# Performance work log

Measured on AMD Instinct MI355X. Metric: run time of the kernel, lower is better.

The kernel has to match this reference:

```python
import jax, jax.numpy as jnp
import numpy as np

REMOVE_FACTOR = 1000000.0


def setup_inputs() -> dict:
    key = jax.random.key(0)
    ks = jax.random.split(key, 6)
    B, Te, Td = 4, 512, 128
    D_en, D_de, U = 256, 512, 128
    en_seq = jax.random.normal(ks[0], (B, Te, D_en), dtype=jnp.float32)
    de_seq = jax.random.normal(ks[1], (B, Td, D_de), dtype=jnp.float32)
    mask = jax.random.randint(ks[2], (B, Te), 0, 2).astype(jnp.int32)
    w_en = jax.random.normal(ks[3], (D_en, U), dtype=jnp.float32) * (1.0 / np.sqrt(D_en))
    w_de = jax.random.normal(ks[4], (D_de, U), dtype=jnp.float32) * (1.0 / np.sqrt(D_de))
    nu = jax.random.normal(ks[5], (U, 1), dtype=jnp.float32) * (1.0 / np.sqrt(U))
    return {"en_seq": en_seq, "de_seq": de_seq, "mask": mask,
            "w_en": w_en, "w_de": w_de, "nu": nu}


def reference(en_seq, de_seq, mask, w_en, w_de, nu):
    # en_seq: [B,Te,D_en], de_seq: [B,Td,D_de], mask: [B,Te] (0/1)
    m = mask.astype(en_seq.dtype)
    en = en_seq * m[..., None]                         # masked encoder states
    en_p = jnp.einsum('bte,eu->btu', en, w_en)          # [B,Te,U]
    de_p = jnp.einsum('bdf,fu->bdu', de_seq, w_de)      # [B,Td,U]
    # additive (Bahdanau) scores: scores[b,td,te] = tanh(en_p[te]+de_p[td]) @ nu
    h = jnp.tanh(en_p[:, None, :, :] + de_p[:, :, None, :])  # [B,Td,Te,U]
    mu = jnp.einsum('bdtu,u->bdt', h, nu[:, 0])               # [B,Td,Te]
    mu = mu + (m[:, None, :] - 1.0) * REMOVE_FACTOR           # mask bias
    alphas = jax.nn.softmax(mu, axis=-1)                      # softmax over Te
    sum_en = jnp.einsum('bdt,btc->bdc', alphas, en)           # [B,Td,D_en]
    return jnp.concatenate([de_seq, sum_en], axis=-1)         # [B,Td,D_de+D_en]
```

## Files before the change

### kernel.cpp

```cpp
#include <hip/hip_runtime.h>

namespace {
constexpr int B = 4, Te = 512, Td = 128, Den = 256, Dde = 512, U = 128;
constexpr float REMOVE = 1000000.0f;
constexpr float L2E2 = 2.885390081777927f;

__device__ __forceinline__ unsigned short f2bf(float f) {
  unsigned u = __float_as_uint(f);
  u += 0x7FFFu + ((u >> 16) & 1u);
  return (unsigned short)(u >> 16);
}
__device__ __forceinline__ float bf2f(unsigned short h) {
  return __uint_as_float(((unsigned)h) << 16);
}
__device__ __forceinline__ void tanh_fma(float ep, float dv, float nv, float& acc) {
  float e = __builtin_amdgcn_exp2f((ep + dv) * L2E2);
  float r = __builtin_amdgcn_rcpf(e + 1.0f);
  acc = fmaf(fmaf(-2.0f, r, 1.0f), nv, acc);
}
__device__ __forceinline__ void fma4(const float4& w, float x, float* a) {
  a[0] = fmaf(x, w.x, a[0]); a[1] = fmaf(x, w.y, a[1]);
  a[2] = fmaf(x, w.z, a[2]); a[3] = fmaf(x, w.w, a[3]);
}

__global__ __launch_bounds__(256) void proj_kernel(
    const float* __restrict__ en_seq, const float* __restrict__ de_seq,
    const int* __restrict__ mask, const float* __restrict__ w_en,
    const float* __restrict__ w_de, unsigned short* __restrict__ en_pT,
    unsigned short* __restrict__ en_bf, float* __restrict__ de_pA,
    float* __restrict__ de_pB, float* __restrict__ out) {
  __shared__ float xs[4096];
  const int blk = blockIdx.x, tid = threadIdx.x;

  if (blk < 128) {
    const int r0 = blk * 16;
    for (int i = tid; i < 1024; i += 256) {
      int row = i >> 6, c4 = i & 63;
      float m = (float)mask[r0 + row];
      float4 v = *(const float4*)(en_seq + (size_t)(r0 + row) * Den + c4 * 4);
      v.x *= m; v.y *= m; v.z *= m; v.w *= m;
      *(float4*)(xs + row * 256 + c4 * 4) = v;
      ushort4 h; h.x = f2bf(v.x); h.y = f2bf(v.y); h.z = f2bf(v.z); h.w = f2bf(v.w);
      *(ushort4*)(en_bf + (size_t)(r0 + row) * Den + c4 * 4) = h;
    }
    __syncthreads();
    const int rg = tid >> 4, ug = tid & 15, u0 = ug * 8;
    float acc[8] = {0, 0, 0, 0, 0, 0, 0, 0};
#pragma unroll 2
    for (int k = 0; k < 256; k += 4) {
      const float* wp = w_en + (size_t)k * U + u0;
      float4 wa0 = *(const float4*)(wp),         wb0 = *(const float4*)(wp + 4);
      float4 wa1 = *(const float4*)(wp + U),     wb1 = *(const float4*)(wp + U + 4);
      float4 wa2 = *(const float4*)(wp + 2 * U), wb2 = *(const float4*)(wp + 2 * U + 4);
      float4 wa3 = *(const float4*)(wp + 3 * U), wb3 = *(const float4*)(wp + 3 * U + 4);
      float4 xv = *(const float4*)(xs + rg * 256 + k);
      fma4(wa0, xv.x, acc); fma4(wb0, xv.x, acc + 4);
      fma4(wa1, xv.y, acc); fma4(wb1, xv.y, acc + 4);
      fma4(wa2, xv.z, acc); fma4(wb2, xv.z, acc + 4);
      fma4(wa3, xv.w, acc); fma4(wb3, xv.w, acc + 4);
    }
    __syncthreads();
    *(float4*)(xs + rg * 128 + u0)     = make_float4(acc[0], acc[1], acc[2], acc[3]);
    *(float4*)(xs + rg * 128 + u0 + 4) = make_float4(acc[4], acc[5], acc[6], acc[7]);
    __syncthreads();
    {
      int r = tid >> 4, uo = (tid & 15) * 8;
      const float* p = xs + r * 128 + uo;
      ushort4 h0, h1;
      h0.x = f2bf(p[0]); h0.y = f2bf(p[1]); h0.z = f2bf(p[2]); h0.w = f2bf(p[3]);
      h1.x = f2bf(p[4]); h1.y = f2bf(p[5]); h1.z = f2bf(p[6]); h1.w = f2bf(p[7]);
      int b = r0 >> 9, teT = (r0 >> 6) & 7, tein0 = r0 & 63;
      unsigned short* dst =
          en_pT + ((size_t)(b * 8 + teT) * 64 + tein0 + r) * U + uo;
      *(ushort4*)dst = h0;
      *(ushort4*)(dst + 4) = h1;
    }
  } else {
    const int q = blk - 128, rt = q >> 1, kh = q & 1;
    const int r0 = rt * 8, k0 = kh * 256;
    for (int i = tid; i < 512; i += 256) {
      int row = i >> 6, c4 = i & 63;
      float4 v = *(const float4*)(de_seq + (size_t)(r0 + row) * Dde + k0 + c4 * 4);
      *(float4*)(xs + row * 256 + c4 * 4) = v;
      *(float4*)(out + (size_t)(r0 + row) * 768 + k0 + c4 * 4) = v;
    }
    __syncthreads();
    const int rg = tid >> 5, ug = tid & 31, u0 = ug * 4;
    float acc[4] = {0, 0, 0, 0};
#pragma unroll 4
    for (int k = 0; k < 256; k += 4) {
      const float* wp = w_de + (size_t)(k0 + k) * U + u0;
      float4 w0 = *(const float4*)(wp);
      float4 w1 = *(const float4*)(wp + U);
      float4 w2 = *(const float4*)(wp + 2 * U);
      float4 w3 = *(const float4*)(wp + 3 * U);
      float4 xv = *(const float4*)(xs + rg * 256 + k);
      fma4(w0, xv.x, acc); fma4(w1, xv.y, acc);
      fma4(w2, xv.z, acc); fma4(w3, xv.w, acc);
    }
    float* dst = kh ? de_pB : de_pA;
    *(float4*)(dst + (size_t)(r0 + rg) * U + u0) =
        make_float4(acc[0], acc[1], acc[2], acc[3]);
  }
}

__global__ __launch_bounds__(256) void score_kernel(
    const unsigned short* __restrict__ en_pT, const float* __restrict__ de_pA,
    const float* __restrict__ de_pB, const float* __restrict__ nu,
    const int* __restrict__ mask, float* __restrict__ mu) {
  __shared__ float tile[64 * 128];
  __shared__ float dep[8 * 128];
  __shared__ float nus[128];
  const int blk = blockIdx.x, tid = threadIdx.x;
  const int teT = blk & 7, tdT = (blk >> 3) & 15, b = blk >> 7;
  const int te0 = teT * 64, td0 = tdT * 8;

  const unsigned short* src = en_pT + (size_t)(b * 8 + teT) * 64 * U;
#pragma unroll
  for (int j = 0; j < 4; ++j) {
    int unit = j * 256 + tid;
    int te = unit >> 4, u0 = (unit & 15) * 8;
    ushort4 ha = *(const ushort4*)(src + (size_t)te * U + u0);
    ushort4 hb = *(const ushort4*)(src + (size_t)te * U + u0 + 4);
    int sw = te & 31;
    float4 f0 = make_float4(bf2f(ha.x), bf2f(ha.y), bf2f(ha.z), bf2f(ha.w));
    float4 f1 = make_float4(bf2f(hb.x), bf2f(hb.y), bf2f(hb.z), bf2f(hb.w));
    *(float4*)(tile + te * 128 + (((u0 >> 2) + 0) ^ sw) * 4) = f0;
    *(float4*)(tile + te * 128 + (((u0 >> 2) + 1) ^ sw) * 4) = f1;
  }
  {
    int row = tid >> 5, qq = tid & 31;
    float4 a = *(const float4*)(de_pA + (size_t)(b * Td + td0 + row) * U + qq * 4);
    float4 c = *(const float4*)(de_pB + (size_t)(b * Td + td0 + row) * U + qq * 4);
    *(float4*)(dep + row * 128 + qq * 4) =
        make_float4(a.x + c.x, a.y + c.y, a.z + c.z, a.w + c.w);
    if (tid < 32) *(float4*)(nus + tid * 4) = *(const float4*)(nu + tid * 4);
  }
  __syncthreads();

  const int te = tid & 63, tdq = tid >> 6, sw = te & 31;
  const float4* trow = (const float4*)(tile + te * 128);
  const float* d0 = dep + (tdq * 2 + 0) * 128;
  const float* d1 = dep + (tdq * 2 + 1) * 128;
  float s0 = 0.f, s1 = 0.f;
#pragma unroll 4
  for (int q = 0; q < 32; ++q) {
    float4 ev = trow[q ^ sw];
    float4 av = *(const float4*)(d0 + q * 4);
    float4 bv = *(const float4*)(d1 + q * 4);
    float4 nv = *(const float4*)(nus + q * 4);
    tanh_fma(ev.x, av.x, nv.x, s0); tanh_fma(ev.x, bv.x, nv.x, s1);
    tanh_fma(ev.y, av.y, nv.y, s0); tanh_fma(ev.y, bv.y, nv.y, s1);
    tanh_fma(ev.z, av.z, nv.z, s0); tanh_fma(ev.z, bv.z, nv.z, s1);
    tanh_fma(ev.w, av.w, nv.w, s0); tanh_fma(ev.w, bv.w, nv.w, s1);
  }
  const int gte = te0 + te;
  float bias = ((float)mask[b * Te + gte] - 1.0f) * REMOVE;
  mu[(size_t)(b * Td + td0 + tdq * 2 + 0) * Te + gte] = s0 + bias;
  mu[(size_t)(b * Td + td0 + tdq * 2 + 1) * Te + gte] = s1 + bias;
}

__global__ __launch_bounds__(512) void out_kernel(
    const unsigned short* __restrict__ en_bf, const int* __restrict__ mask,
    const float* __restrict__ mu, float* __restrict__ out) {
  __shared__ float al[Te * 4];
  __shared__ float part[8 * 4 * 128];
  const int blk = blockIdx.x, tid = threadIdx.x;
  const int chH = blk & 1, tdT = (blk >> 1) & 31, b = blk >> 6;
  const int td0 = tdT * 4;
  const int wid = tid >> 6, lane = tid & 63;

  if (wid < 4) {
    const float* murow = mu + (size_t)(b * Td + td0 + wid) * Te;
    const int* mrow = mask + b * Te;
    float v[8]; float mx = -3.0e38f;
#pragma unroll
    for (int i = 0; i < 8; ++i) { v[i] = murow[lane + i * 64]; mx = fmaxf(mx, v[i]); }
#pragma unroll
    for (int o = 32; o >= 1; o >>= 1) mx = fmaxf(mx, __shfl_xor(mx, o));
    float ss = 0.f;
#pragma unroll
    for (int i = 0; i < 8; ++i) { v[i] = __expf(v[i] - mx); ss += v[i]; }
#pragma unroll
    for (int o = 32; o >= 1; o >>= 1) ss += __shfl_xor(ss, o);
    float inv = 1.0f / ss;
#pragma unroll
    for (int i = 0; i < 8; ++i) {
      int te = lane + i * 64;
      al[te * 4 + wid] = v[i] * inv * (float)mrow[te];
    }
  }
  __syncthreads();

  {
    const int c0 = chH * 128 + lane * 2;
    const unsigned short* eb = en_bf + (size_t)b * Te * Den + c0;
    float a00 = 0, a01 = 0, a10 = 0, a11 = 0, a20 = 0, a21 = 0, a30 = 0, a31 = 0;
#pragma unroll 4
    for (int t = 0; t < 64; ++t) {
      int te = wid * 64 + t;
      ushort2 h = *(const ushort2*)(eb + (size_t)te * Den);
      float4 av = *(const float4*)(al + te * 4);
      float e0 = bf2f(h.x), e1 = bf2f(h.y);
      a00 = fmaf(av.x, e0, a00); a01 = fmaf(av.x, e1, a01);
      a10 = fmaf(av.y, e0, a10); a11 = fmaf(av.y, e1, a11);
      a20 = fmaf(av.z, e0, a20); a21 = fmaf(av.z, e1, a21);
      a30 = fmaf(av.w, e0, a30); a31 = fmaf(av.w, e1, a31);
    }
    *(float2*)(part + (wid * 4 + 0) * 128 + lane * 2) = make_float2(a00, a01);
    *(float2*)(part + (wid * 4 + 1) * 128 + lane * 2) = make_float2(a10, a11);
    *(float2*)(part + (wid * 4 + 2) * 128 + lane * 2) = make_float2(a20, a21);
    *(float2*)(part + (wid * 4 + 3) * 128 + lane * 2) = make_float2(a30, a31);
  }
  __syncthreads();

  {
    int td = tid >> 7, cc = tid & 127;
    float r = 0.f;
#pragma unroll
    for (int w = 0; w < 8; ++w) r += part[(w * 4 + td) * 128 + cc];
    out[(size_t)(b * Td + td0 + td) * 768 + 512 + chH * 128 + cc] = r;
  }
}
}

extern "C" void kernel_launch(void* const* d_in, const int* in_sizes, int n_in,
                              void* d_out, int out_size, void* d_ws, size_t ws_size,
                              hipStream_t stream) {
  const float* en_seq = (const float*)d_in[0];
  const float* de_seq = (const float*)d_in[1];
  const int*   mask   = (const int*)d_in[2];
  const float* w_en   = (const float*)d_in[3];
  const float* w_de   = (const float*)d_in[4];
  const float* nu     = (const float*)d_in[5];
  float* out = (float*)d_out;

  unsigned short* en_pT = (unsigned short*)d_ws;
  unsigned short* en_bf = en_pT + (size_t)B * Te * U;
  float* de_pA = (float*)(en_bf + (size_t)B * Te * Den);
  float* de_pB = de_pA + (size_t)B * Td * U;
  float* mu    = de_pB + (size_t)B * Td * U;

  hipLaunchKernelGGL(proj_kernel, dim3(256), dim3(256), 0, stream,
                     en_seq, de_seq, mask, w_en, w_de, en_pT, en_bf,
                     de_pA, de_pB, out);
  hipLaunchKernelGGL(score_kernel, dim3(512), dim3(256), 0, stream,
                     en_pT, de_pA, de_pB, nu, mask, mu);
  hipLaunchKernelGGL(out_kernel, dim3(256), dim3(512), 0, stream,
                     en_bf, mask, mu, out);
}
```

Before: 41.01 us.

## Transpose encoder projection layout and restructure score and output kernels

Stores the projected encoder tile as U-major (transposed) so the score kernel can read contiguous te-vectors. Each thread now computes a 4x4 te-by-td register block over a slice of U, followed by a shared-memory reduction across U slices. The score grid doubles to 1024 blocks with 4 td rows per block. The projection kernel uses 8-row blocks, giving more blocks. The output kernel covers all 256 channels for 2 td rows per block instead of splitting channels. The aim is better data reuse and occupancy in the tanh-heavy score stage, at the cost of an extra reduction pass and more blocks.

New measurement: 43.28 us. +5.5%, slower.

```diff
diff --git a/kernel.cpp b/kernel.cpp
--- a/kernel.cpp
+++ b/kernel.cpp
@@ -29,12 +29,12 @@
     const float* __restrict__ w_de, unsigned short* __restrict__ en_pT,
     unsigned short* __restrict__ en_bf, float* __restrict__ de_pA,
     float* __restrict__ de_pB, float* __restrict__ out) {
-  __shared__ float xs[4096];
+  __shared__ float xs[2048];
   const int blk = blockIdx.x, tid = threadIdx.x;
 
-  if (blk < 128) {
-    const int r0 = blk * 16;
-    for (int i = tid; i < 1024; i += 256) {
+  if (blk < 256) {
+    const int r0 = blk * 8;
+    for (int i = tid; i < 512; i += 256) {
       int row = i >> 6, c4 = i & 63;
       float m = (float)mask[r0 + row];
       float4 v = *(const float4*)(en_seq + (size_t)(r0 + row) * Den + c4 * 4);
@@ -44,39 +44,34 @@
       *(ushort4*)(en_bf + (size_t)(r0 + row) * Den + c4 * 4) = h;
     }
     __syncthreads();
-    const int rg = tid >> 4, ug = tid & 15, u0 = ug * 8;
-    float acc[8] = {0, 0, 0, 0, 0, 0, 0, 0};
-#pragma unroll 2
+    const int rg = tid >> 5, ug = tid & 31, u0 = ug * 4;
+    float acc[4] = {0, 0, 0, 0};
+#pragma unroll 4
     for (int k = 0; k < 256; k += 4) {
       const float* wp = w_en + (size_t)k * U + u0;
-      float4 wa0 = *(const float4*)(wp),         wb0 = *(const float4*)(wp + 4);
-      float4 wa1 = *(const float4*)(wp + U),     wb1 = *(const float4*)(wp + U + 4);
-      float4 wa2 = *(const float4*)(wp + 2 * U), wb2 = *(const float4*)(wp + 2 * U + 4);
-      float4 wa3 = *(const float4*)(wp + 3 * U), wb3 = *(const float4*)(wp + 3 * U + 4);
+      float4 w0 = *(const float4*)(wp);
+      float4 w1 = *(const float4*)(wp + U);
+      float4 w2 = *(const float4*)(wp + 2 * U);
+      float4 w3 = *(const float4*)(wp + 3 * U);
       float4 xv = *(const float4*)(xs + rg * 256 + k);
-      fma4(wa0, xv.x, acc); fma4(wb0, xv.x, acc + 4);
-      fma4(wa1, xv.y, acc); fma4(wb1, xv.y, acc + 4);
-      fma4(wa2, xv.z, acc); fma4(wb2, xv.z, acc + 4);
-      fma4(wa3, xv.w, acc); fma4(wb3, xv.w, acc + 4);
-    }
-    __syncthreads();
-    *(float4*)(xs + rg * 128 + u0)     = make_float4(acc[0], acc[1], acc[2], acc[3]);
-    *(float4*)(xs + rg * 128 + u0 + 4) = make_float4(acc[4], acc[5], acc[6], acc[7]);
+      fma4(w0, xv.x, acc); fma4(w1, xv.y, acc);
+      fma4(w2, xv.z, acc); fma4(w3, xv.w, acc);
+    }
+    __syncthreads();
+    *(float4*)(xs + rg * 128 + u0) = make_float4(acc[0], acc[1], acc[2], acc[3]);
     __syncthreads();
     {
-      int r = tid >> 4, uo = (tid & 15) * 8;
-      const float* p = xs + r * 128 + uo;
-      ushort4 h0, h1;
-      h0.x = f2bf(p[0]); h0.y = f2bf(p[1]); h0.z = f2bf(p[2]); h0.w = f2bf(p[3]);
-      h1.x = f2bf(p[4]); h1.y = f2bf(p[5]); h1.z = f2bf(p[6]); h1.w = f2bf(p[7]);
+      int u = tid >> 1, half = tid & 1;
+      ushort4 h;
+      h.x = f2bf(xs[(half * 4 + 0) * 128 + u]);
+      h.y = f2bf(xs[(half * 4 + 1) * 128 + u]);
+      h.z = f2bf(xs[(half * 4 + 2) * 128 + u]);
+      h.w = f2bf(xs[(half * 4 + 3) * 128 + u]);
       int b = r0 >> 9, teT = (r0 >> 6) & 7, tein0 = r0 & 63;
-      unsigned short* dst =
-          en_pT + ((size_t)(b * 8 + teT) * 64 + tein0 + r) * U + uo;
-      *(ushort4*)dst = h0;
-      *(ushort4*)(dst + 4) = h1;
+      *(ushort4*)(en_pT + ((size_t)(b * 8 + teT) * 128 + u) * 64 + tein0 + half * 4) = h;
     }
   } else {
-    const int q = blk - 128, rt = q >> 1, kh = q & 1;
+    const int q = blk - 256, rt = q >> 1, kh = q & 1;
     const int r0 = rt * 8, k0 = kh * 256;
     for (int i = tid; i < 512; i += 256) {
       int row = i >> 6, c4 = i & 63;
@@ -104,74 +99,89 @@
   }
 }
 
-__global__ __launch_bounds__(256) void score_kernel(
+__global__ __launch_bounds__(256, 4) void score_kernel(
     const unsigned short* __restrict__ en_pT, const float* __restrict__ de_pA,
     const float* __restrict__ de_pB, const float* __restrict__ nu,
     const int* __restrict__ mask, float* __restrict__ mu) {
-  __shared__ float tile[64 * 128];
-  __shared__ float dep[8 * 128];
+  __shared__ float tileT[128 * 64];
+  __shared__ float depT[128 * 4];
   __shared__ float nus[128];
   const int blk = blockIdx.x, tid = threadIdx.x;
-  const int teT = blk & 7, tdT = (blk >> 3) & 15, b = blk >> 7;
-  const int te0 = teT * 64, td0 = tdT * 8;
-
-  const unsigned short* src = en_pT + (size_t)(b * 8 + teT) * 64 * U;
+  const int teT = blk & 7, tdT = (blk >> 3) & 31, b = blk >> 8;
+  const int te0 = teT * 64, td0 = tdT * 4;
+
+  const unsigned short* src = en_pT + (size_t)(b * 8 + teT) * 128 * 64;
 #pragma unroll
   for (int j = 0; j < 4; ++j) {
     int unit = j * 256 + tid;
-    int te = unit >> 4, u0 = (unit & 15) * 8;
-    ushort4 ha = *(const ushort4*)(src + (size_t)te * U + u0);
-    ushort4 hb = *(const ushort4*)(src + (size_t)te * U + u0 + 4);
-    int sw = te & 31;
-    float4 f0 = make_float4(bf2f(ha.x), bf2f(ha.y), bf2f(ha.z), bf2f(ha.w));
-    float4 f1 = make_float4(bf2f(hb.x), bf2f(hb.y), bf2f(hb.z), bf2f(hb.w));
-    *(float4*)(tile + te * 128 + (((u0 >> 2) + 0) ^ sw) * 4) = f0;
-    *(float4*)(tile + te * 128 + (((u0 >> 2) + 1) ^ sw) * 4) = f1;
-  }
-  {
-    int row = tid >> 5, qq = tid & 31;
-    float4 a = *(const float4*)(de_pA + (size_t)(b * Td + td0 + row) * U + qq * 4);
-    float4 c = *(const float4*)(de_pB + (size_t)(b * Td + td0 + row) * U + qq * 4);
-    *(float4*)(dep + row * 128 + qq * 4) =
-        make_float4(a.x + c.x, a.y + c.y, a.z + c.z, a.w + c.w);
-    if (tid < 32) *(float4*)(nus + tid * 4) = *(const float4*)(nu + tid * 4);
-  }
-  __syncthreads();
-
-  const int te = tid & 63, tdq = tid >> 6, sw = te & 31;
-  const float4* trow = (const float4*)(tile + te * 128);
-  const float* d0 = dep + (tdq * 2 + 0) * 128;
-  const float* d1 = dep + (tdq * 2 + 1) * 128;
-  float s0 = 0.f, s1 = 0.f;
-#pragma unroll 4
-  for (int q = 0; q < 32; ++q) {
-    float4 ev = trow[q ^ sw];
-    float4 av = *(const float4*)(d0 + q * 4);
-    float4 bv = *(const float4*)(d1 + q * 4);
-    float4 nv = *(const float4*)(nus + q * 4);
-    tanh_fma(ev.x, av.x, nv.x, s0); tanh_fma(ev.x, bv.x, nv.x, s1);
-    tanh_fma(ev.y, av.y, nv.y, s0); tanh_fma(ev.y, bv.y, nv.y, s1);
-    tanh_fma(ev.z, av.z, nv.z, s0); tanh_fma(ev.z, bv.z, nv.z, s1);
-    tanh_fma(ev.w, av.w, nv.w, s0); tanh_fma(ev.w, bv.w, nv.w, s1);
-  }
-  const int gte = te0 + te;
-  float bias = ((float)mask[b * Te + gte] - 1.0f) * REMOVE;
-  mu[(size_t)(b * Td + td0 + tdq * 2 + 0) * Te + gte] = s0 + bias;
-  mu[(size_t)(b * Td + td0 + tdq * 2 + 1) * Te + gte] = s1 + bias;
+    int u = unit >> 3, tc = (unit & 7) * 8;
+    ushort4 ha = *(const ushort4*)(src + (size_t)u * 64 + tc);
+    ushort4 hb = *(const ushort4*)(src + (size_t)u * 64 + tc + 4);
+    *(float4*)(tileT + u * 64 + tc) =
+        make_float4(bf2f(ha.x), bf2f(ha.y), bf2f(ha.z), bf2f(ha.w));
+    *(float4*)(tileT + u * 64 + tc + 4) =
+        make_float4(bf2f(hb.x), bf2f(hb.y), bf2f(hb.z), bf2f(hb.w));
+  }
+  for (int i = tid; i < 512; i += 256) {
+    int u = i & 127, td = i >> 7;
+    float v = de_pA[((size_t)b * Td + td0 + td) * U + u] +
+              de_pB[((size_t)b * Td + td0 + td) * U + u];
+    depT[u * 4 + td] = v;
+  }
+  if (tid < 128) nus[tid] = nu[tid];
+  __syncthreads();
+
+  const int tp = tid & 15, us = tid >> 4;
+  const int tel0 = tp * 4;
+  float a00=0,a01=0,a02=0,a03=0, a10=0,a11=0,a12=0,a13=0;
+  float a20=0,a21=0,a22=0,a23=0, a30=0,a31=0,a32=0,a33=0;
+#pragma unroll
+  for (int jj = 0; jj < 8; ++jj) {
+    int u = us + 16 * jj;
+    float4 ev = *(const float4*)(tileT + u * 64 + tel0);
+    float4 dv = *(const float4*)(depT + u * 4);
+    float nv = nus[u];
+    tanh_fma(ev.x, dv.x, nv, a00); tanh_fma(ev.y, dv.x, nv, a01);
+    tanh_fma(ev.z, dv.x, nv, a02); tanh_fma(ev.w, dv.x, nv, a03);
+    tanh_fma(ev.x, dv.y, nv, a10); tanh_fma(ev.y, dv.y, nv, a11);
+    tanh_fma(ev.z, dv.y, nv, a12); tanh_fma(ev.w, dv.y, nv, a13);
+    tanh_fma(ev.x, dv.z, nv, a20); tanh_fma(ev.y, dv.z, nv, a21);
+    tanh_fma(ev.z, dv.z, nv, a22); tanh_fma(ev.w, dv.z, nv, a23);
+    tanh_fma(ev.x, dv.w, nv, a30); tanh_fma(ev.y, dv.w, nv, a31);
+    tanh_fma(ev.z, dv.w, nv, a32); tanh_fma(ev.w, dv.w, nv, a33);
+  }
+  __syncthreads();
+  float* scr = tileT;
+  {
+    float* p = scr + us * 256 + tel0;
+    p[0]   = a00; p[1]   = a01; p[2]   = a02; p[3]   = a03;
+    p[64]  = a10; p[65]  = a11; p[66]  = a12; p[67]  = a13;
+    p[128] = a20; p[129] = a21; p[130] = a22; p[131] = a23;
+    p[192] = a30; p[193] = a31; p[194] = a32; p[195] = a33;
+  }
+  __syncthreads();
+  {
+    int td = tid >> 6, te = tid & 63;
+    float s = 0.f;
+#pragma unroll
+    for (int q = 0; q < 16; ++q) s += scr[q * 256 + tid];
+    float bias = ((float)mask[b * Te + te0 + te] - 1.0f) * REMOVE;
+    mu[((size_t)b * Td + td0 + td) * Te + te0 + te] = s + bias;
+  }
 }
 
 __global__ __launch_bounds__(512) void out_kernel(
     const unsigned short* __restrict__ en_bf, const int* __restrict__ mask,
     const float* __restrict__ mu, float* __restrict__ out) {
-  __shared__ float al[Te * 4];
-  __shared__ float part[8 * 4 * 128];
+  __shared__ float al[Te * 2];
+  __shared__ float scr[8 * 2 * 256];
   const int blk = blockIdx.x, tid = threadIdx.x;
-  const int chH = blk & 1, tdT = (blk >> 1) & 31, b = blk >> 6;
-  const int td0 = tdT * 4;
+  const int b = blk >> 6, tdT = blk & 63;
+  const int gtd0 = b * Td + tdT * 2;
   const int wid = tid >> 6, lane = tid & 63;
 
-  if (wid < 4) {
-    const float* murow = mu + (size_t)(b * Td + td0 + wid) * Te;
+  if (wid < 2) {
+    const float* murow = mu + (size_t)(gtd0 + wid) * Te;
     const int* mrow = mask + b * Te;
     float v[8]; float mx = -3.0e38f;
 #pragma unroll
@@ -187,39 +197,37 @@
 #pragma unroll
     for (int i = 0; i < 8; ++i) {
       int te = lane + i * 64;
-      al[te * 4 + wid] = v[i] * inv * (float)mrow[te];
-    }
-  }
-  __syncthreads();
-
-  {
-    const int c0 = chH * 128 + lane * 2;
+      al[te * 2 + wid] = v[i] * inv * (float)mrow[te];
+    }
+  }
+  __syncthreads();
+
+  {
+    const int c0 = lane * 4;
     const unsigned short* eb = en_bf + (size_t)b * Te * Den + c0;
-    float a00 = 0, a01 = 0, a10 = 0, a11 = 0, a20 = 0, a21 = 0, a30 = 0, a31 = 0;
+    float p0[4] = {0, 0, 0, 0}, p1[4] = {0, 0, 0, 0};
 #pragma unroll 4
     for (int t = 0; t < 64; ++t) {
       int te = wid * 64 + t;
-      ushort2 h = *(const ushort2*)(eb + (size_t)te * Den);
-      float4 av = *(const float4*)(al + te * 4);
-      float e0 = bf2f(h.x), e1 = bf2f(h.y);
-      a00 = fmaf(av.x, e0, a00); a01 = fmaf(av.x, e1, a01);
-      a10 = fmaf(av.y, e0, a10); a11 = fmaf(av.y, e1, a11);
-      a20 = fmaf(av.z, e0, a20); a21 = fmaf(av.z, e1, a21);
-      a30 = fmaf(av.w, e0, a30); a31 = fmaf(av.w, e1, a31);
-    }
-    *(float2*)(part + (wid * 4 + 0) * 128 + lane * 2) = make_float2(a00, a01);
-    *(float2*)(part + (wid * 4 + 1) * 128 + lane * 2) = make_float2(a10, a11);
-    *(float2*)(part + (wid * 4 + 2) * 128 + lane * 2) = make_float2(a20, a21);
-    *(float2*)(part + (wid * 4 + 3) * 128 + lane * 2) = make_float2(a30, a31);
-  }
-  __syncthreads();
-
-  {
-    int td = tid >> 7, cc = tid & 127;
+      ushort4 h = *(const ushort4*)(eb + (size_t)te * Den);
+      float2 av = *(const float2*)(al + te * 2);
+      float e0 = bf2f(h.x), e1 = bf2f(h.y), e2 = bf2f(h.z), e3 = bf2f(h.w);
+      p0[0] = fmaf(av.x, e0, p0[0]); p0[1] = fmaf(av.x, e1, p0[1]);
+      p0[2] = fmaf(av.x, e2, p0[2]); p0[3] = fmaf(av.x, e3, p0[3]);
+      p1[0] = fmaf(av.y, e0, p1[0]); p1[1] = fmaf(av.y, e1, p1[1]);
+      p1[2] = fmaf(av.y, e2, p1[2]); p1[3] = fmaf(av.y, e3, p1[3]);
+    }
+    *(float4*)(scr + (wid * 2 + 0) * 256 + c0) = make_float4(p0[0], p0[1], p0[2], p0[3]);
+    *(float4*)(scr + (wid * 2 + 1) * 256 + c0) = make_float4(p1[0], p1[1], p1[2], p1[3]);
+  }
+  __syncthreads();
+
+  {
+    int td = tid >> 8, ch = tid & 255;
     float r = 0.f;
 #pragma unroll
-    for (int w = 0; w < 8; ++w) r += part[(w * 4 + td) * 128 + cc];
-    out[(size_t)(b * Td + td0 + td) * 768 + 512 + chH * 128 + cc] = r;
+    for (int w = 0; w < 8; ++w) r += scr[(w * 2 + td) * 256 + ch];
+    out[(size_t)(gtd0 + td) * 768 + 512 + ch] = r;
   }
 }
 }
@@ -241,10 +249,10 @@
   float* de_pB = de_pA + (size_t)B * Td * U;
   float* mu    = de_pB + (size_t)B * Td * U;
 
-  hipLaunchKernelGGL(proj_kernel, dim3(256), dim3(256), 0, stream,
+  hipLaunchKernelGGL(proj_kernel, dim3(384), dim3(256), 0, stream,
                      en_seq, de_seq, mask, w_en, w_de, en_pT, en_bf,
                      de_pA, de_pB, out);
-  hipLaunchKernelGGL(score_kernel, dim3(512), dim3(256), 0, stream,
+  hipLaunchKernelGGL(score_kernel, dim3(1024), dim3(256), 0, stream,
                      en_pT, de_pA, de_pB, nu, mask, mu);
   hipLaunchKernelGGL(out_kernel, dim3(256), dim3(512), 0, stream,
                      en_bf, mask, mu, out);
```
